# Optimization experiments

Measured on AMD Instinct MI355X. Metric: run time of the kernel, lower is better.

Reference implementation:

```python
import jax, jax.numpy as jnp
import numpy as np


def lrelu(x):
    return jnp.where(x > 0, x, 0.1 * x)


def setup_inputs() -> dict:
    key = jax.random.key(0)
    ks = jax.random.split(key, 16)
    L, B, E = 160, 16, 512
    C, H, DM, DO = 256, 512, 128, 512  # conv channels, enc_hid, d_mlp, dec_hid

    def rn(k, shape, scale=0.05):
        return jax.random.normal(k, shape, dtype=jnp.float32) * scale

    return {
        "x": rn(ks[0], (L, B, E), 1.0),
        "h": rn(ks[1], (B, H), 1.0),
        "conv_w": rn(ks[2], (C, E, 3)),
        "conv_b": rn(ks[3], (C,)),
        "bn_g": jnp.ones((C,), jnp.float32),
        "bn_b": jnp.zeros((C,), jnp.float32),
        "W1": rn(ks[4], (DM, 2 * (C + 2) + H)),
        "b1": rn(ks[5], (DM,)),
        "W2": rn(ks[6], (DM, DM)), "b2": rn(ks[7], (DM,)),
        "W3": rn(ks[8], (DM, DM)), "b3": rn(ks[9], (DM,)),
        "W4": rn(ks[10], (DM, DM)), "b4": rn(ks[11], (DM,)),
        "W5": rn(ks[12], (DM, DM)), "b5": rn(ks[13], (DM,)),
        "W6": rn(ks[14], (DO, DM)), "b6": rn(ks[15], (DO,)),
    }


def reference(x, h, conv_w, conv_b, bn_g, bn_b,
              W1, b1, W2, b2, W3, b3, W4, b4, W5, b5, W6, b6):
    L, B, E = x.shape
    # --- ConvLayer: Conv1d(k=3, pad=1) -> LeakyReLU(0.1) -> BatchNorm1d (training stats)
    xc = jnp.transpose(x, (1, 2, 0))  # (B, E, L)
    y = jax.lax.conv_general_dilated(xc, conv_w, (1,), [(1, 1)],
                                     dimension_numbers=("NCH", "OIH", "NCH"))
    y = lrelu(y + conv_b[None, :, None])
    mu = y.mean(axis=(0, 2), keepdims=True)
    var = y.var(axis=(0, 2), keepdims=True)  # biased variance (torch training BN)
    y = (y - mu) * jax.lax.rsqrt(var + 1e-5)
    y = y * bn_g[None, :, None] + bn_b[None, :, None]
    y = jnp.transpose(y, (0, 2, 1))  # (B, L, C)

    # --- coordinate features: [(i/sqrt(L)-2)/2, (i % sqrt(L) - 2)/2]
    sL = np.sqrt(L)
    i = jnp.arange(L, dtype=jnp.float32)
    coords = jnp.stack([(i / sL - 2.0) / 2.0, (jnp.mod(i, sL) - 2.0) / 2.0], axis=-1)  # (L, 2)
    xf = jnp.concatenate([y, jnp.broadcast_to(coords[None], (B, L, 2))], axis=-1)  # (B, L, C+2)
    Cp = xf.shape[-1]

    # --- g_mlp first Linear decomposed over [x_i | x_j | h] feature blocks:
    # x_i[b,a,c] = xf[b,c] (varies with dim2); x_j[b,a,c] = cat(xf[b,a], h[b]) (varies with dim1)
    W1i = W1[:, :Cp]            # acts on x_i
    W1jx = W1[:, Cp:2 * Cp]     # acts on x part of x_j
    W1jh = W1[:, 2 * Cp:]       # acts on h part of x_j
    u = jnp.einsum('blc,dc->bld', xf, W1i)                     # (B, L, DM), index = dim2
    v = jnp.einsum('blc,dc->bld', xf, W1jx) + (h @ W1jh.T)[:, None, :]  # (B, L, DM), index = dim1
    z = lrelu(v[:, :, None, :] + u[:, None, :, :] + b1)        # (B, L, L, DM)
    z = lrelu(z @ W2.T + b2)
    z = lrelu(z @ W3.T + b3)
    z = lrelu(z @ W4.T + b4)
    s = z.sum(axis=(1, 2))  # sum over all L*L pairs -> (B, DM)

    # --- f_mlp
    s = lrelu(s @ W5.T + b5)
    return lrelu(s @ W6.T + b6)  # (B, dec_hid)
```

## Files before the change

### kernel.cpp

```cpp
#include <hip/hip_runtime.h>
#include <cstdint>

typedef unsigned short u16;
typedef uint32_t u32;

typedef __bf16 bf16x8 __attribute__((ext_vector_type(8)));
typedef float  f32x2  __attribute__((ext_vector_type(2)));
typedef float  f32x4  __attribute__((ext_vector_type(4)));
typedef float  f32x16 __attribute__((ext_vector_type(16)));
typedef u16    u16x4  __attribute__((ext_vector_type(4)));
typedef u16    u16x8  __attribute__((ext_vector_type(8)));

__device__ __forceinline__ u16 f2bf(float f) {
    u32 x = __float_as_uint(f);
    return (u16)((x + 0x7FFFu + ((x >> 16) & 1u)) >> 16);
}
__device__ __forceinline__ float lrelu(float x) { return fmaxf(x, 0.1f * x); }

__device__ __forceinline__ u32 pack_rn(float lo, float hi) {
    u32 a = __float_as_uint(lo) + 0x8000u;
    u32 b = __float_as_uint(hi) + 0x8000u;
    return __builtin_amdgcn_perm(b, a, 0x07060302u);
}

__global__ __launch_bounds__(256) void k_prep(
    const float* __restrict__ x, const float* __restrict__ conv_w,
    const float* __restrict__ W2, const float* __restrict__ W3, const float* __restrict__ W4,
    const float* __restrict__ b2, const float* __restrict__ b3, const float* __restrict__ b4,
    const float* __restrict__ h, const float* __restrict__ W1,
    u16* __restrict__ xb, u16* __restrict__ wcb, u16* __restrict__ wfrag,
    float* __restrict__ hW)
{
    int blk = blockIdx.x, tid = threadIdx.x;
    if (blk < 1280) {
        int o = (blk * 256 + tid) * 4;
        int e = o & 511;
        int bl = o >> 9;
        int b = bl / 160, l = bl % 160;
        f32x4 v = *(const f32x4*)(x + ((size_t)(l * 16 + b)) * 512 + e);
        u16x4 ov;
        ov[0] = f2bf(v[0]); ov[1] = f2bf(v[1]); ov[2] = f2bf(v[2]); ov[3] = f2bf(v[3]);
        *(u16x4*)&xb[o] = ov;
    } else if (blk < 1664) {
        int o = ((blk - 1280) * 256 + tid) * 4;
        int c = o / 1536, rem = o % 1536;
        int t = rem >> 9, e0 = rem & 511;
        u16x4 ov;
        #pragma unroll
        for (int q = 0; q < 4; q++)
            ov[q] = f2bf(conv_w[((size_t)c * 512 + e0 + q) * 3 + t]);
        *(u16x4*)&wcb[o] = ov;
    } else if (blk < 1718) {
        int o = ((blk - 1664) * 256 + tid) * 4;
        int layer = o / 18432, rem = o % 18432;
        int ks9 = rem >> 11;
        int rem2 = rem & 2047;
        int hh = rem2 >> 10;
        int rem3 = rem2 & 1023;
        int n = rem3 >> 3, j0 = rem3 & 7;
        const float* W = (layer == 0) ? W2 : (layer == 1) ? W3 : W4;
        const float* bi = (layer == 0) ? b2 : (layer == 1) ? b3 : b4;
        u16x4 ov;
        if (ks9 < 8) {
            f32x4 v = *(const f32x4*)(W + (size_t)n * 128 + 16 * ks9 + 8 * hh + j0);
            ov[0] = f2bf(v[0]); ov[1] = f2bf(v[1]); ov[2] = f2bf(v[2]); ov[3] = f2bf(v[3]);
        } else {
            ov[0] = (hh == 0 && j0 == 0) ? f2bf(bi[n]) : (u16)0;
            ov[1] = 0; ov[2] = 0; ov[3] = 0;
        }
        *(u16x4*)&wfrag[o] = ov;
    } else {
        int gid = (blk - 1718) * 256 + tid;
        int outp = gid >> 4, q = gid & 15;
        int b = outp >> 7, d = outp & 127;
        const float* hr = h + (size_t)b * 512;
        const float* wr = W1 + (size_t)d * 1028 + 516;
        float acc = 0.f;
        #pragma unroll
        for (int c = 0; c < 8; c++) {
            int k = c * 64 + q * 4;
            f32x4 hv = *(const f32x4*)(hr + k);
            f32x4 wv = *(const f32x4*)(wr + k);
            acc += hv[0]*wv[0] + hv[1]*wv[1] + hv[2]*wv[2] + hv[3]*wv[3];
        }
        acc += __shfl_xor(acc, 1); acc += __shfl_xor(acc, 2);
        acc += __shfl_xor(acc, 4); acc += __shfl_xor(acc, 8);
        if (q == 0) hW[outp] = acc;
    }
}

__global__ __launch_bounds__(256, 2) void k_conv(
    const u16* __restrict__ xb, const u16* __restrict__ wcb,
    const float* __restrict__ conv_b,
    float* __restrict__ ws_y, float* __restrict__ stats)
{
    __shared__ u16 xs[34 * 520];
    int tid = threadIdx.x, wg = blockIdx.x;
    int rowtile = wg >> 2, cg = wg & 3;
    int b = rowtile / 5, l0 = (rowtile % 5) * 32;

    for (int t = tid; t < 34 * 64; t += 256) {
        int s = t >> 6, ch = t & 63;
        int lg = l0 + s - 1;
        u16x8 v = {};
        if (lg >= 0 && lg < 160)
            v = *(const u16x8*)(xb + ((size_t)(b * 160 + lg)) * 512 + ch * 8);
        *(u16x8*)&xs[s * 520 + ch * 8] = v;
    }
    __syncthreads();

    int lane = tid & 63, w = tid >> 6;
    int row16 = lane & 15, quad = lane >> 4;
    int c_n = cg * 64 + w * 16 + row16;
    const u16* wrow = wcb + (size_t)c_n * 1536;

    f32x4 acc0 = {0,0,0,0}, acc1 = {0,0,0,0};
    for (int ks4 = 0; ks4 < 48; ks4 += 4) {
        bf16x8 wf[4];
        #pragma unroll
        for (int q = 0; q < 4; q++)
            wf[q] = *(const bf16x8*)(wrow + (ks4 + q) * 32 + quad * 8);
        #pragma unroll
        for (int q = 0; q < 4; q++) {
            int k = (ks4 + q) * 32 + quad * 8;
            int tap = k >> 9, e = k & 511;
            bf16x8 a0 = *(const bf16x8*)&xs[(row16 + tap) * 520 + e];
            bf16x8 a1 = *(const bf16x8*)&xs[(16 + row16 + tap) * 520 + e];
            acc0 = __builtin_amdgcn_mfma_f32_16x16x32_bf16(a0, wf[q], acc0, 0, 0, 0);
            acc1 = __builtin_amdgcn_mfma_f32_16x16x32_bf16(a1, wf[q], acc1, 0, 0, 0);
        }
    }

    float bias = conv_b[c_n];
    float sum = 0.f, sq = 0.f;
    #pragma unroll
    for (int mt = 0; mt < 2; mt++) {
        f32x4 a = mt ? acc1 : acc0;
        #pragma unroll
        for (int r = 0; r < 4; r++) {
            float v = lrelu(a[r] + bias);
            int lr = l0 + mt * 16 + quad * 4 + r;
            ws_y[((size_t)(b * 160 + lr)) * 256 + c_n] = v;
            sum += v; sq += v * v;
        }
    }
    sum += __shfl_xor(sum, 16); sum += __shfl_xor(sum, 32);
    sq  += __shfl_xor(sq, 16);  sq  += __shfl_xor(sq, 32);
    if (quad == 0) {
        atomicAdd(&stats[c_n], sum);
        atomicAdd(&stats[256 + c_n], sq);
    }
}

__global__ __launch_bounds__(256) void k_uv(
    const float* __restrict__ ws_y, const float* __restrict__ stats,
    const float* __restrict__ bn_g, const float* __restrict__ bn_b,
    const float* __restrict__ W1, const float* __restrict__ b1,
    const float* __restrict__ hW,
    float* __restrict__ uu, float* __restrict__ vv)
{
    __shared__ float a_s[256], c_s[256];
    __shared__ float xfs[8 * 260];
    int tid = threadIdx.x;
    int row0 = blockIdx.x * 8;
    int b = row0 / 160, l0 = row0 % 160;
    {
        int c = tid;
        float mu  = stats[c] * (1.0f / 2560.0f);
        float var = stats[256 + c] * (1.0f / 2560.0f) - mu * mu;
        float rs  = rsqrtf(var + 1e-5f) * bn_g[c];
        a_s[c] = rs;
        c_s[c] = bn_b[c] - mu * rs;
    }
    __syncthreads();
    float sLf = sqrtf(160.0f);
    for (int idx = tid; idx < 8 * 258; idx += 256) {
        int r = idx / 258, c = idx - r * 258;
        int l = l0 + r;
        float v;
        if (c < 256) {
            v = ws_y[((size_t)(b * 160 + l)) * 256 + c] * a_s[c] + c_s[c];
        } else {
            float fi = (float)l;
            if (c == 256) v = (fi / sLf - 2.0f) * 0.5f;
            else { float m = fi - floorf(fi / sLf) * sLf; v = (m - 2.0f) * 0.5f; }
        }
        xfs[r * 260 + c] = v;
    }
    __syncthreads();

    bool isv = tid >= 128;
    int d = tid & 127;
    const float* wrow = W1 + (size_t)d * 1028 + (isv ? 258 : 0);

    float acc[8] = {0,0,0,0,0,0,0,0};
    for (int c0 = 0; c0 < 256; c0 += 32) {
        f32x4 wv[8];
        #pragma unroll
        for (int q = 0; q < 8; q++)
            wv[q] = *(const f32x4*)(wrow + c0 + q * 4);
        #pragma unroll
        for (int q = 0; q < 8; q++) {
            #pragma unroll
            for (int r = 0; r < 8; r++) {
                f32x4 xv = *(const f32x4*)&xfs[r * 260 + c0 + q * 4];
                acc[r] += wv[q][0]*xv[0] + wv[q][1]*xv[1] + wv[q][2]*xv[2] + wv[q][3]*xv[3];
            }
        }
    }
    float w256 = wrow[256], w257 = wrow[257];
    #pragma unroll
    for (int r = 0; r < 8; r++)
        acc[r] += xfs[r * 260 + 256] * w256 + xfs[r * 260 + 257] * w257;

    float vadd = isv ? (hW[b * 128 + d] + b1[d]) : 0.f;
    float* dst = isv ? vv : uu;
    #pragma unroll
    for (int r = 0; r < 8; r++)
        dst[((size_t)(b * 160 + l0 + r)) * 128 + d] = acc[r] + vadd;
}

__global__ __launch_bounds__(256, 4) void k_mlp(
    const float* __restrict__ vv, const float* __restrict__ uu,
    const u16* __restrict__ wfrag,
    float* __restrict__ s_glob)
{
    __shared__ __align__(16) u16 Wlds[18432];
    __shared__ float spart[128];
    int tid = threadIdx.x;
    int wave = tid >> 6, lane = tid & 63;
    int h = lane >> 5, lo = lane & 31;
    int b = blockIdx.x / 200, sub = blockIdx.x % 200;
    int tileb = sub * 4 + wave;

    if (tid < 128) spart[tid] = 0.f;

    u32 selv = h ? 0x07060302u : 0x05040100u;
    uint4 biasfrag;
    biasfrag.x = (h == 0) ? 0x00003F80u : 0u;
    biasfrag.y = 0u; biasfrag.z = 0u; biasfrag.w = 0u;

    f32x16 Z;
    #pragma unroll
    for (int r = 0; r < 16; r++) Z[r] = 0.f;

    uint4 B[8], Bn[8];
    float ssum[4];

    int i  = (tileb / 10) * 2  + (lo >> 4);
    int jj = (tileb % 10) * 16 + (lo & 15);
    const float* vr = vv + ((size_t)(b * 160 + i))  * 128 + 8 * h;
    const float* ur = uu + ((size_t)(b * 160 + jj)) * 128 + 8 * h;

    for (int layer = 0; layer < 3; layer++) {
        __syncthreads();
        {
            const uint4* src = (const uint4*)(wfrag + layer * 18432);
            #pragma unroll
            for (int it = 0; it < 9; it++) {
                int idx = it * 256 + tid;
                *(uint4*)&Wlds[idx * 8] = src[idx];
            }
        }
        __syncthreads();

        if (layer == 0) {
            #pragma unroll
            for (int ks = 0; ks < 8; ks++) {
                f32x4 v0 = *(const f32x4*)(vr + 16 * ks);
                f32x4 v1 = *(const f32x4*)(vr + 16 * ks + 4);
                f32x4 u0 = *(const f32x4*)(ur + 16 * ks);
                f32x4 u1 = *(const f32x4*)(ur + 16 * ks + 4);
                uint4 d;
                d.x = pack_rn(lrelu(v0[0]+u0[0]), lrelu(v0[1]+u0[1]));
                d.y = pack_rn(lrelu(v0[2]+u0[2]), lrelu(v0[3]+u0[3]));
                d.z = pack_rn(lrelu(v1[0]+u1[0]), lrelu(v1[1]+u1[1]));
                d.w = pack_rn(lrelu(v1[2]+u1[2]), lrelu(v1[3]+u1[3]));
                B[ks] = d;
            }
        }

        #pragma unroll
        for (int nt = 0; nt < 4; nt++) {
            f32x16 a;
            #pragma unroll
            for (int ks = 0; ks < 9; ks++) {
                bf16x8 wf = *(const bf16x8*)&Wlds[(size_t)(ks * 256 + h * 128 + nt * 32 + lo) * 8];
                uint4 zu = (ks < 8) ? B[ks] : biasfrag;
                bf16x8 zf = *(bf16x8*)&zu;
                if (layer < 2)
                    a = __builtin_amdgcn_mfma_f32_32x32x16_bf16(wf, zf, ks ? a : Z, 0, 0, 0);
                else
                    a = __builtin_amdgcn_mfma_f32_32x32x16_bf16(zf, wf, ks ? a : Z, 0, 0, 0);
            }

            if (layer < 2) {
                u32 pk[4][2];
                #pragma unroll
                for (int c = 0; c < 4; c++)
                    #pragma unroll
                    for (int p = 0; p < 2; p++)
                        pk[c][p] = pack_rn(lrelu(a[c + 8*p]),
                                           lrelu(a[c + 4 + 8*p]));
                u32 sh[2][4][2];
                #pragma unroll
                for (int g = 0; g < 2; g++)
                    #pragma unroll
                    for (int c = 0; c < 4; c++)
                        #pragma unroll
                        for (int p = 0; p < 2; p++)
                            sh[g][c][p] = (u32)__shfl((int)pk[c][p], g * 32 + lo, 64);
                #pragma unroll
                for (int p = 0; p < 2; p++) {
                    uint4 d;
                    d.x = __builtin_amdgcn_perm(sh[0][1][p], sh[0][0][p], selv);
                    d.y = __builtin_amdgcn_perm(sh[0][3][p], sh[0][2][p], selv);
                    d.z = __builtin_amdgcn_perm(sh[1][1][p], sh[1][0][p], selv);
                    d.w = __builtin_amdgcn_perm(sh[1][3][p], sh[1][2][p], selv);
                    Bn[2 * nt + p] = d;
                }
            } else {
                float t = 0.f;
                #pragma unroll
                for (int r = 0; r < 16; r++)
                    t += lrelu(a[r]);
                ssum[nt] = t;
            }
        }

        if (layer < 2) {
            #pragma unroll
            for (int ks = 0; ks < 8; ks++) B[ks] = Bn[ks];
        }
    }

    #pragma unroll
    for (int nt = 0; nt < 4; nt++) {
        float v = ssum[nt] + __shfl_xor(ssum[nt], 32);
        if (h == 0) atomicAdd(&spart[nt * 32 + lo], v);
    }
    __syncthreads();
    if (tid < 128) atomicAdd(&s_glob[b * 128 + tid], spart[tid]);
}

__global__ __launch_bounds__(256) void k_final(
    const float* __restrict__ s_glob,
    const float* __restrict__ W5, const float* __restrict__ b5,
    const float* __restrict__ W6, const float* __restrict__ b6,
    float* __restrict__ out)
{
    __shared__ float sh[128], t5[128];
    int b = blockIdx.x, tid = threadIdx.x;
    if (tid < 128) sh[tid] = s_glob[b * 128 + tid];
    __syncthreads();
    if (tid < 128) {
        const float* wr = W5 + (size_t)tid * 128;
        float acc = b5[tid];
        #pragma unroll
        for (int k = 0; k < 128; k += 4) {
            f32x4 wv = *(const f32x4*)(wr + k);
            f32x4 sv = *(const f32x4*)&sh[k];
            acc += wv[0]*sv[0] + wv[1]*sv[1] + wv[2]*sv[2] + wv[3]*sv[3];
        }
        t5[tid] = lrelu(acc);
    }
    __syncthreads();
    #pragma unroll
    for (int q = 0; q < 2; q++) {
        int o = q * 256 + tid;
        const float* wr = W6 + (size_t)o * 128;
        float acc = b6[o];
        #pragma unroll
        for (int k = 0; k < 128; k += 4) {
            f32x4 wv = *(const f32x4*)(wr + k);
            f32x4 tv = *(const f32x4*)&t5[k];
            acc += wv[0]*tv[0] + wv[1]*tv[1] + wv[2]*tv[2] + wv[3]*tv[3];
        }
        out[b * 512 + o] = lrelu(acc);
    }
}

extern "C" void kernel_launch(void* const* d_in, const int* in_sizes, int n_in,
                              void* d_out, int out_size, void* d_ws, size_t ws_size,
                              hipStream_t stream)
{
    const float* x      = (const float*)d_in[0];
    const float* h      = (const float*)d_in[1];
    const float* conv_w = (const float*)d_in[2];
    const float* conv_b = (const float*)d_in[3];
    const float* bn_g   = (const float*)d_in[4];
    const float* bn_b   = (const float*)d_in[5];
    const float* W1     = (const float*)d_in[6];
    const float* b1     = (const float*)d_in[7];
    const float* W2     = (const float*)d_in[8];
    const float* b2     = (const float*)d_in[9];
    const float* W3     = (const float*)d_in[10];
    const float* b3     = (const float*)d_in[11];
    const float* W4     = (const float*)d_in[12];
    const float* b4     = (const float*)d_in[13];
    const float* W5     = (const float*)d_in[14];
    const float* b5     = (const float*)d_in[15];
    const float* W6     = (const float*)d_in[16];
    const float* b6     = (const float*)d_in[17];

    char* ws = (char*)d_ws;
    float* s_glob = (float*)(ws + 0);
    float* stats  = (float*)(ws + 8192);
    float* hW     = (float*)(ws + 10240);
    float* ws_y   = (float*)(ws + 18432);
    float* vv     = (float*)(ws + 2639872);
    float* uu     = (float*)(ws + 3950592);
    u16*   xb     = (u16*)  (ws + 5261312);
    u16*   wcb    = (u16*)  (ws + 7882752);
    u16*   wfrag  = (u16*)  (ws + 8669184);

    hipMemsetAsync(ws, 0, 10240, stream);
    k_prep <<<1846, 256, 0, stream>>>(x, conv_w, W2, W3, W4, b2, b3, b4, h, W1,
                                      xb, wcb, wfrag, hW);
    k_conv <<<320, 256, 0, stream>>>(xb, wcb, conv_b, ws_y, stats);
    k_uv   <<<320, 256, 0, stream>>>(ws_y, stats, bn_g, bn_b, W1, b1, hW, uu, vv);
    k_mlp  <<<3200, 256, 0, stream>>>(vv, uu, wfrag, s_glob);
    k_final<<<16, 256, 0, stream>>>(s_glob, W5, b5, W6, b6, (float*)d_out);
}
```

Measured before the change: 209.5 us.

## Pre-swizzle conv and W1 weights, widen MLP blocks, simplify lane exchange

Conv weights are now prepacked in MFMA fragment order so each lane's load is contiguous. W1 is transposed into a float4-interleaved layout so k_uv reads coalesced weights. k_mlp moves to 512-thread blocks (8 waves) so each staged weight load into LDS is shared by more tiles. Its output re-layout now uses one xor-shuffle plus selects instead of two indexed shuffles. Together these cut uncoalesced loads, weight staging and shuffle count, at the cost of more prep work and a larger block that may lower occupancy.

```diff
diff --git a/kernel.cpp b/kernel.cpp
--- a/kernel.cpp
+++ b/kernel.cpp
@@ -28,8 +28,8 @@
     const float* __restrict__ W2, const float* __restrict__ W3, const float* __restrict__ W4,
     const float* __restrict__ b2, const float* __restrict__ b3, const float* __restrict__ b4,
     const float* __restrict__ h, const float* __restrict__ W1,
-    u16* __restrict__ xb, u16* __restrict__ wcb, u16* __restrict__ wfrag,
-    float* __restrict__ hW)
+    u16* __restrict__ xb, u16* __restrict__ wcb_f, u16* __restrict__ wfrag,
+    float* __restrict__ W1T4, float* __restrict__ hW)
 {
     int blk = blockIdx.x, tid = threadIdx.x;
     if (blk < 1280) {
@@ -41,17 +41,22 @@
         u16x4 ov;
         ov[0] = f2bf(v[0]); ov[1] = f2bf(v[1]); ov[2] = f2bf(v[2]); ov[3] = f2bf(v[3]);
         *(u16x4*)&xb[o] = ov;
-    } else if (blk < 1664) {
-        int o = ((blk - 1280) * 256 + tid) * 4;
-        int c = o / 1536, rem = o % 1536;
-        int t = rem >> 9, e0 = rem & 511;
-        u16x4 ov;
-        #pragma unroll
-        for (int q = 0; q < 4; q++)
-            ov[q] = f2bf(conv_w[((size_t)c * 512 + e0 + q) * 3 + t]);
-        *(u16x4*)&wcb[o] = ov;
-    } else if (blk < 1718) {
-        int o = ((blk - 1664) * 256 + tid) * 4;
+    } else if (blk < 1472) {
+        int g = (blk - 1280) * 256 + tid;
+        int lane = g & 63;
+        int ks = (g >> 6) % 48;
+        int cb = g / 3072;
+        int c = cb * 16 + (lane & 15);
+        int quad = lane >> 4;
+        int k0 = ks * 32 + quad * 8;
+        int tap = k0 >> 9, e0 = k0 & 511;
+        u16x8 ov;
+        #pragma unroll
+        for (int j = 0; j < 8; j++)
+            ov[j] = f2bf(conv_w[((size_t)c * 512 + e0 + j) * 3 + tap]);
+        *(u16x8*)&wcb_f[(size_t)g * 8] = ov;
+    } else if (blk < 1526) {
+        int o = ((blk - 1472) * 256 + tid) * 4;
         int layer = o / 18432, rem = o % 18432;
         int ks9 = rem >> 11;
         int rem2 = rem & 2047;
@@ -69,8 +74,21 @@
             ov[1] = 0; ov[2] = 0; ov[3] = 0;
         }
         *(u16x4*)&wfrag[o] = ov;
+    } else if (blk < 1591) {
+        int cq = blk - 1526;
+        int t = tid;
+        const float* src = (t < 128)
+            ? (W1 + (size_t)t * 1028 + cq * 4)
+            : (W1 + (size_t)(t - 128) * 1028 + 258 + cq * 4);
+        f32x2 v0 = *(const f32x2*)src;
+        f32x2 v1 = *(const f32x2*)(src + 2);
+        f32x4 v;
+        v[0] = v0[0]; v[1] = v0[1];
+        v[2] = (cq == 64) ? 0.f : v1[0];
+        v[3] = (cq == 64) ? 0.f : v1[1];
+        *(f32x4*)&W1T4[((size_t)cq * 256 + t) * 4] = v;
     } else {
-        int gid = (blk - 1718) * 256 + tid;
+        int gid = (blk - 1591) * 256 + tid;
         int outp = gid >> 4, q = gid & 15;
         int b = outp >> 7, d = outp & 127;
         const float* hr = h + (size_t)b * 512;
@@ -90,7 +108,7 @@
 }
 
 __global__ __launch_bounds__(256, 2) void k_conv(
-    const u16* __restrict__ xb, const u16* __restrict__ wcb,
+    const u16* __restrict__ xb, const u16* __restrict__ wcb_f,
     const float* __restrict__ conv_b,
     float* __restrict__ ws_y, float* __restrict__ stats)
 {
@@ -111,15 +129,16 @@
 
     int lane = tid & 63, w = tid >> 6;
     int row16 = lane & 15, quad = lane >> 4;
-    int c_n = cg * 64 + w * 16 + row16;
-    const u16* wrow = wcb + (size_t)c_n * 1536;
+    int cb = cg * 4 + w;
+    int c_n = cb * 16 + row16;
+    const u16* wb = wcb_f + (size_t)cb * 24576;
 
     f32x4 acc0 = {0,0,0,0}, acc1 = {0,0,0,0};
     for (int ks4 = 0; ks4 < 48; ks4 += 4) {
         bf16x8 wf[4];
         #pragma unroll
         for (int q = 0; q < 4; q++)
-            wf[q] = *(const bf16x8*)(wrow + (ks4 + q) * 32 + quad * 8);
+            wf[q] = *(const bf16x8*)(wb + (size_t)((ks4 + q) * 64 + lane) * 8);
         #pragma unroll
         for (int q = 0; q < 4; q++) {
             int k = (ks4 + q) * 32 + quad * 8;
@@ -155,7 +174,7 @@
 __global__ __launch_bounds__(256) void k_uv(
     const float* __restrict__ ws_y, const float* __restrict__ stats,
     const float* __restrict__ bn_g, const float* __restrict__ bn_b,
-    const float* __restrict__ W1, const float* __restrict__ b1,
+    const float* __restrict__ W1T4, const float* __restrict__ b1,
     const float* __restrict__ hW,
     float* __restrict__ uu, float* __restrict__ vv)
 {
@@ -174,45 +193,36 @@
     }
     __syncthreads();
     float sLf = sqrtf(160.0f);
-    for (int idx = tid; idx < 8 * 258; idx += 256) {
-        int r = idx / 258, c = idx - r * 258;
+    for (int idx = tid; idx < 8 * 260; idx += 256) {
+        int r = idx / 260, c = idx - r * 260;
         int l = l0 + r;
-        float v;
+        float v = 0.f;
         if (c < 256) {
             v = ws_y[((size_t)(b * 160 + l)) * 256 + c] * a_s[c] + c_s[c];
-        } else {
+        } else if (c == 256) {
+            v = ((float)l / sLf - 2.0f) * 0.5f;
+        } else if (c == 257) {
             float fi = (float)l;
-            if (c == 256) v = (fi / sLf - 2.0f) * 0.5f;
-            else { float m = fi - floorf(fi / sLf) * sLf; v = (m - 2.0f) * 0.5f; }
+            float m = fi - floorf(fi / sLf) * sLf;
+            v = (m - 2.0f) * 0.5f;
         }
         xfs[r * 260 + c] = v;
     }
     __syncthreads();
+
+    float acc[8] = {0,0,0,0,0,0,0,0};
+    #pragma unroll 4
+    for (int cq = 0; cq < 65; cq++) {
+        f32x4 w4 = *(const f32x4*)&W1T4[((size_t)cq * 256 + tid) * 4];
+        #pragma unroll
+        for (int r = 0; r < 8; r++) {
+            f32x4 xv = *(const f32x4*)&xfs[r * 260 + cq * 4];
+            acc[r] += w4[0]*xv[0] + w4[1]*xv[1] + w4[2]*xv[2] + w4[3]*xv[3];
+        }
+    }
 
     bool isv = tid >= 128;
     int d = tid & 127;
-    const float* wrow = W1 + (size_t)d * 1028 + (isv ? 258 : 0);
-
-    float acc[8] = {0,0,0,0,0,0,0,0};
-    for (int c0 = 0; c0 < 256; c0 += 32) {
-        f32x4 wv[8];
-        #pragma unroll
-        for (int q = 0; q < 8; q++)
-            wv[q] = *(const f32x4*)(wrow + c0 + q * 4);
-        #pragma unroll
-        for (int q = 0; q < 8; q++) {
-            #pragma unroll
-            for (int r = 0; r < 8; r++) {
-                f32x4 xv = *(const f32x4*)&xfs[r * 260 + c0 + q * 4];
-                acc[r] += wv[q][0]*xv[0] + wv[q][1]*xv[1] + wv[q][2]*xv[2] + wv[q][3]*xv[3];
-            }
-        }
-    }
-    float w256 = wrow[256], w257 = wrow[257];
-    #pragma unroll
-    for (int r = 0; r < 8; r++)
-        acc[r] += xfs[r * 260 + 256] * w256 + xfs[r * 260 + 257] * w257;
-
     float vadd = isv ? (hW[b * 128 + d] + b1[d]) : 0.f;
     float* dst = isv ? vv : uu;
     #pragma unroll
@@ -220,7 +230,7 @@
         dst[((size_t)(b * 160 + l0 + r)) * 128 + d] = acc[r] + vadd;
 }
 
-__global__ __launch_bounds__(256, 4) void k_mlp(
+__global__ __launch_bounds__(512, 4) void k_mlp(
     const float* __restrict__ vv, const float* __restrict__ uu,
     const u16* __restrict__ wfrag,
     float* __restrict__ s_glob)
@@ -230,8 +240,8 @@
     int tid = threadIdx.x;
     int wave = tid >> 6, lane = tid & 63;
     int h = lane >> 5, lo = lane & 31;
-    int b = blockIdx.x / 200, sub = blockIdx.x % 200;
-    int tileb = sub * 4 + wave;
+    int b = blockIdx.x / 100, sub = blockIdx.x % 100;
+    int tileb = sub * 8 + wave;
 
     if (tid < 128) spart[tid] = 0.f;
 
@@ -257,9 +267,10 @@
         {
             const uint4* src = (const uint4*)(wfrag + layer * 18432);
             #pragma unroll
-            for (int it = 0; it < 9; it++) {
-                int idx = it * 256 + tid;
-                *(uint4*)&Wlds[idx * 8] = src[idx];
+            for (int it = 0; it < 5; it++) {
+                int idx = it * 512 + tid;
+                if (idx < 2304)
+                    *(uint4*)&Wlds[idx * 8] = src[idx];
             }
         }
         __syncthreads();
@@ -295,28 +306,29 @@
             }
 
             if (layer < 2) {
-                u32 pk[4][2];
+                u32 own[4][2], oth[4][2];
                 #pragma unroll
                 for (int c = 0; c < 4; c++)
                     #pragma unroll
                     for (int p = 0; p < 2; p++)
-                        pk[c][p] = pack_rn(lrelu(a[c + 8*p]),
-                                           lrelu(a[c + 4 + 8*p]));
-                u32 sh[2][4][2];
+                        own[c][p] = pack_rn(lrelu(a[c + 8*p]),
+                                            lrelu(a[c + 4 + 8*p]));
                 #pragma unroll
-                for (int g = 0; g < 2; g++)
+                for (int c = 0; c < 4; c++)
                     #pragma unroll
-                    for (int c = 0; c < 4; c++)
-                        #pragma unroll
-                        for (int p = 0; p < 2; p++)
-                            sh[g][c][p] = (u32)__shfl((int)pk[c][p], g * 32 + lo, 64);
+                    for (int p = 0; p < 2; p++)
+                        oth[c][p] = (u32)__shfl_xor((int)own[c][p], 32);
                 #pragma unroll
                 for (int p = 0; p < 2; p++) {
+                    u32 dA0 = __builtin_amdgcn_perm(own[1][p], own[0][p], selv);
+                    u32 dB0 = __builtin_amdgcn_perm(oth[1][p], oth[0][p], selv);
+                    u32 dA1 = __builtin_amdgcn_perm(own[3][p], own[2][p], selv);
+                    u32 dB1 = __builtin_amdgcn_perm(oth[3][p], oth[2][p], selv);
                     uint4 d;
-                    d.x = __builtin_amdgcn_perm(sh[0][1][p], sh[0][0][p], selv);
-                    d.y = __builtin_amdgcn_perm(sh[0][3][p], sh[0][2][p], selv);
-                    d.z = __builtin_amdgcn_perm(sh[1][1][p], sh[1][0][p], selv);
-                    d.w = __builtin_amdgcn_perm(sh[1][3][p], sh[1][2][p], selv);
+                    d.x = h ? dB0 : dA0;
+                    d.y = h ? dB1 : dA1;
+                    d.z = h ? dA0 : dB0;
+                    d.w = h ? dA1 : dB1;
                     Bn[2 * nt + p] = d;
                 }
             } else {
@@ -411,14 +423,15 @@
     float* vv     = (float*)(ws + 2639872);
     float* uu     = (float*)(ws + 3950592);
     u16*   xb     = (u16*)  (ws + 5261312);
-    u16*   wcb    = (u16*)  (ws + 7882752);
+    u16*   wcb_f  = (u16*)  (ws + 7882752);
     u16*   wfrag  = (u16*)  (ws + 8669184);
+    float* W1T4   = (float*)(ws + 8779776);
 
     hipMemsetAsync(ws, 0, 10240, stream);
-    k_prep <<<1846, 256, 0, stream>>>(x, conv_w, W2, W3, W4, b2, b3, b4, h, W1,
-                                      xb, wcb, wfrag, hW);
-    k_conv <<<320, 256, 0, stream>>>(xb, wcb, conv_b, ws_y, stats);
-    k_uv   <<<320, 256, 0, stream>>>(ws_y, stats, bn_g, bn_b, W1, b1, hW, uu, vv);
-    k_mlp  <<<3200, 256, 0, stream>>>(vv, uu, wfrag, s_glob);
+    k_prep <<<1719, 256, 0, stream>>>(x, conv_w, W2, W3, W4, b2, b3, b4, h, W1,
+                                      xb, wcb_f, wfrag, W1T4, hW);
+    k_conv <<<320, 256, 0, stream>>>(xb, wcb_f, conv_b, ws_y, stats);
+    k_uv   <<<320, 256, 0, stream>>>(ws_y, stats, bn_g, bn_b, W1T4, b1, hW, uu, vv);
+    k_mlp  <<<1600, 512, 0, stream>>>(vv, uu, wfrag, s_glob);
     k_final<<<16, 256, 0, stream>>>(s_glob, W5, b5, W6, b6, (float*)d_out);
 }
```

Result: slower. 215.5 us (+2.9%).
